# Performance work log

Measured on AMD Instinct MI355X. Metric: run time of the kernel, lower is better.

## Reference

```python
import jax, jax.numpy as jnp
import numpy as np

KMAX = 16
NEG_INF = -1e9


def setup_inputs() -> dict:
    key = jax.random.key(0)
    ks = jax.random.split(key, 8)
    B, N, H = 65536, 512, 256
    L = KMAX + 1
    actions = jax.random.randint(ks[0], (B, L), 0, N + 1)  # values in [0, N], N == STOP
    rp = jax.random.uniform(ks[1], (B, 1), dtype=jnp.float32)
    s1 = 1.0 / np.sqrt(N + 3)
    s2 = 1.0 / np.sqrt(H)
    W1 = jax.random.normal(ks[2], (N + 3, H), dtype=jnp.float32) * s1
    b1 = jax.random.normal(ks[3], (H,), dtype=jnp.float32) * 0.01
    W2 = jax.random.normal(ks[4], (H, H), dtype=jnp.float32) * s2
    b2 = jax.random.normal(ks[5], (H,), dtype=jnp.float32) * 0.01
    Wh = jax.random.normal(ks[6], (H, N + 1), dtype=jnp.float32) * s2
    bh = jax.random.normal(ks[7], (N + 1,), dtype=jnp.float32) * 0.01
    return {"actions": actions, "rp": rp, "W1": W1, "b1": b1, "W2": W2, "b2": b2, "Wh": Wh, "bh": bh}


def reference(actions, rp, W1, b1, W2, b2, Wh, bh):
    B, L = actions.shape
    N = Wh.shape[1] - 1
    f32 = rp.dtype

    def step_fn(carry, a):
        sel_mask, k_sel, step, logpf = carry  # [B,N], [B,1], [B,1], [B]
        x = jnp.concatenate([sel_mask, k_sel, step, rp], axis=-1)  # [B, N+3]
        h = jax.nn.relu(x @ W1 + b1)
        h = jax.nn.relu(h @ W2 + b2)
        logits = h @ Wh + bh  # [B, N+1]
        k = k_sel[:, 0]
        full = (k >= KMAX).astype(f32)[:, None]
        mask_assets = (1.0 - sel_mask) * (1.0 - full)  # cannot re-add or exceed Kmax
        mask_stop = (k > 0).astype(f32)[:, None]       # cannot STOP on empty set
        mask = jnp.concatenate([mask_assets, mask_stop], axis=-1)
        logits = jnp.where(mask <= 0.0, NEG_INF, logits)
        logp = jax.nn.log_softmax(logits, axis=-1)
        alive = a >= 0
        a_safe = jnp.clip(a, 0, N)
        chosen = jnp.take_along_axis(logp, a_safe[:, None], axis=-1)[:, 0]
        logpf = logpf + jnp.where(alive, chosen, 0.0)
        stop = (a == N) & alive
        add = (alive & (~stop)).astype(f32)[:, None]
        # one_hot of N/-1 is all-zero, so only valid adds update sel_mask
        upd = jax.nn.one_hot(a_safe, N, dtype=f32) * add
        sel_mask = jnp.maximum(sel_mask, upd)
        k_sel = jnp.sum(sel_mask, axis=-1, keepdims=True)
        step = step + 1.0
        return (sel_mask, k_sel, step, logpf), None

    init = (jnp.zeros((B, N), f32), jnp.zeros((B, 1), f32), jnp.zeros((B, 1), f32), jnp.zeros((B,), f32))
    (_, _, _, logpf), _ = jax.lax.scan(step_fn, init, actions.T)  # scan over L steps
    return logpf
```

## Files before the change

kernel.cpp:

```cpp
#include <hip/hip_runtime.h>


#define NEG_INF (-1000000000.0f)
#define LOG2E 1.4426950408889634f
#define LN2   0.6931471805599453f

#define A_NEW  0x400

#define HST 1040
#define HKT 2080

typedef short bf16x8 __attribute__((ext_vector_type(8)));
typedef float f32x16 __attribute__((ext_vector_type(16)));

__device__ __forceinline__ unsigned short f2bf(float x){
  unsigned int u = __float_as_uint(x);
  u = (u + 0x7FFFu + ((u >> 16) & 1u)) >> 16;
  return (unsigned short)u;
}
__device__ __forceinline__ float bf2f(unsigned short h){
  return __uint_as_float(((unsigned int)h) << 16);
}
__device__ __forceinline__ unsigned int cvt_pk_bf16(float lo, float hi){
  unsigned int r;
  asm("v_cvt_pk_bf16_f32 %0, %1, %2" : "=v"(r) : "v"(lo), "v"(hi));
  return r;
}
__device__ __forceinline__ float4 ld4bf(const unsigned short* p){
  ushort4 u = *(const ushort4*)p;
  return make_float4(bf2f(u.x), bf2f(u.y), bf2f(u.z), bf2f(u.w));
}

__global__ void prep_kernel(const float* __restrict__ W2, const float* __restrict__ Wh,
                            unsigned short* __restrict__ w2f, unsigned short* __restrict__ whf,
                            float* __restrict__ whstop){
  int id = blockIdx.x * 256 + threadIdx.x;
  if (id < 8192){
    int lane = id & 63; int tile = id >> 6;
    int ntg = tile & 7, kt = tile >> 3;
    int col = ntg * 32 + (lane & 31);
    int k0  = kt * 16 + (lane >> 5) * 8;
    unsigned int u[4];
#pragma unroll
    for (int p = 0; p < 4; ++p){
      unsigned short lo = f2bf(W2[(k0 + 2*p    ) * 256 + col]);
      unsigned short hi = f2bf(W2[(k0 + 2*p + 1) * 256 + col]);
      u[p] = (unsigned int)lo | ((unsigned int)hi << 16);
    }
    *(uint4*)(w2f + (size_t)id * 8) = make_uint4(u[0], u[1], u[2], u[3]);
  } else if (id < 24576){
    int id2 = id - 8192;
    int lane = id2 & 63; int tile = id2 >> 6;
    int ntg = tile & 15, kt = tile >> 4;
    int col = ntg * 32 + (lane & 31);
    int k0  = kt * 16 + (lane >> 5) * 8;
    unsigned int u[4];
#pragma unroll
    for (int p = 0; p < 4; ++p){
      unsigned short lo = f2bf(Wh[(k0 + 2*p    ) * 513 + col] * LOG2E);
      unsigned short hi = f2bf(Wh[(k0 + 2*p + 1) * 513 + col] * LOG2E);
      u[p] = (unsigned int)lo | ((unsigned int)hi << 16);
    }
    *(uint4*)(whf + (size_t)id2 * 8) = make_uint4(u[0], u[1], u[2], u[3]);
  } else if (id < 24832){
    int k = id - 24576;
    whstop[k] = Wh[k * 513 + 512];
  }
}

__launch_bounds__(256, 3)
__global__ void gfn_kernel(const int* __restrict__ actions, const float* __restrict__ rp,
                           const float* __restrict__ W1, const float* __restrict__ b1,
                           const float* __restrict__ b2, const float* __restrict__ bh,
                           const unsigned short* __restrict__ w2f,
                           const unsigned short* __restrict__ whf,
                           const float* __restrict__ whstop,
                           float* __restrict__ out)
{
  __shared__ alignas(16) char h[32 * HST];
  __shared__ alignas(16) unsigned short c16[1024];
  __shared__ alignas(16) unsigned int selp[16][32];
  __shared__ alignas(16) float bhl2[512];
  __shared__ alignas(16) unsigned short b2s16[256];
  __shared__ alignas(16) unsigned short whst_h[256];
  __shared__ alignas(16) unsigned short amask[18][32];
  __shared__ alignas(16) float pred[64][4];
  __shared__ alignas(16) float stopp[64];
  __shared__ alignas(16) float chosen[64];

  const int tid  = threadIdx.x;
  const int wave = tid >> 6;
  const int lane = tid & 63;
  const int ln5  = lane & 31;
  const int lg2  = lane >> 5;
  const int base = blockIdx.x * 32;

  for (int i = tid; i < 1024; i += 256){
    int rrow = i >> 8, f = i & 255;
    float v = (rrow < 3) ? W1[(512 + rrow) * 256 + f] : b1[f];
    c16[i] = f2bf(v);
  }
  b2s16[tid] = f2bf(b2[tid]);
  whst_h[tid] = f2bf(whstop[tid]);
  for (int i = tid; i < 512; i += 256){
    int pt = i >> 5, l2 = (i >> 4) & 1, r = i & 15;
    int col = pt * 32 + (r & 3) + 8 * (r >> 2) + 4 * l2;
    bhl2[i] = bh[col] * LOG2E;
  }
  const float stopbias = bh[512];
  for (int i = tid; i < 512; i += 256) ((unsigned int*)selp)[i] = 0u;
  if (tid < 64) stopp[tid] = 0.f;
  int* acts = (int*)h;
  for (int i = tid; i < 544; i += 256) acts[i] = actions[base * 17 + i];
  float logpf = 0.f;
  __syncthreads();

  if (tid < 32){
    int s = tid, k = 0;
    for (int t = 0; t < 17; ++t){
      int a = acts[s * 17 + t];
      bool alive = (a >= 0);
      bool isnew = alive && (a < 512);
      if (isnew){
        for (int u = 0; u < t; ++u) if (acts[s * 17 + u] == a){ isnew = false; break; }
      }
      int av = alive ? a : 1023;
      amask[t][s] = (unsigned short)(av | (isnew ? A_NEW : 0) | (k << 11));
      if (isnew) ++k;
    }
    amask[17][s] = (unsigned short)(1023 | (k << 11));
  }
  unsigned int Spk[16];
#pragma unroll
  for (int j = 0; j < 16; ++j) Spk[j] = 0u;
  __syncthreads();

  const int aw_base = (lane >> 1) * HST + (lane & 1) * 8 + wave * 128;
  const int br_base = lg2 * HST;
  const int bw_base = wave * 8 * HST + lg2 * 8;
  const int cr_base = lg2 * HST + ln5 * 16;
  const int rpu = __builtin_amdgcn_readfirstlane(base + wave * 8);

#pragma unroll 1
  for (int c = 0; c < 9; ++c){
    const int t = c * 2;

    {
      const float4 ck4 = ld4bf(&c16[lane * 4]);
      const float4 ct4 = ld4bf(&c16[256 + lane * 4]);
      const float4 cr4 = ld4bf(&c16[512 + lane * 4]);
      const float4 cb4 = ld4bf(&c16[768 + lane * 4]);
      float tf = (float)t;
      float c00 = cb4.x + tf * ct4.x, c01 = cb4.y + tf * ct4.y;
      float c02 = cb4.z + tf * ct4.z, c03 = cb4.w + tf * ct4.w;
#pragma unroll
      for (int s8 = 0; s8 < 8; ++s8){
        int s = wave * 8 + s8;
        float rv = rp[rpu + s8];
        int m0 = amask[t][s];
        int m1 = amask[t + 1][s];
        unsigned int pk0 = Spk[s8 * 2], pk1 = Spk[s8 * 2 + 1];
        float S0 = __uint_as_float(pk0 << 16);
        float S1 = __uint_as_float(pk0 & 0xFFFF0000u);
        float S2 = __uint_as_float(pk1 << 16);
        float S3 = __uint_as_float(pk1 & 0xFFFF0000u);
        float kf = (float)(m0 >> 11);
        float v0 = S0 + kf * ck4.x + rv * cr4.x + c00;
        float v1 = S1 + kf * ck4.y + rv * cr4.y + c01;
        float v2 = S2 + kf * ck4.z + rv * cr4.z + c02;
        float v3 = S3 + kf * ck4.w + rv * cr4.w + c03;
        *(uint2*)(h + aw_base + s8 * 16) =
            make_uint2(cvt_pk_bf16(fmaxf(v0,0.f), fmaxf(v1,0.f)),
                       cvt_pk_bf16(fmaxf(v2,0.f), fmaxf(v3,0.f)));
        float d0 = ct4.x, d1 = ct4.y, d2 = ct4.z, d3 = ct4.w;
        if (m0 & A_NEW){
          int a = m0 & 1023;
          float4 w = *(const float4*)(W1 + (size_t)a * 256 + lane * 4);
          S0 += w.x; S1 += w.y; S2 += w.z; S3 += w.w;
          d0 += w.x + ck4.x; d1 += w.y + ck4.y; d2 += w.z + ck4.z; d3 += w.w + ck4.w;
        }
        v0 += d0; v1 += d1; v2 += d2; v3 += d3;
        *(uint2*)(h + aw_base + 512 + s8 * 16) =
            make_uint2(cvt_pk_bf16(fmaxf(v0,0.f), fmaxf(v1,0.f)),
                       cvt_pk_bf16(fmaxf(v2,0.f), fmaxf(v3,0.f)));
        if (m1 & A_NEW){
          int a = m1 & 1023;
          float4 w = *(const float4*)(W1 + (size_t)a * 256 + lane * 4);
          S0 += w.x; S1 += w.y; S2 += w.z; S3 += w.w;
        }
        if ((m0 | m1) & A_NEW){
          Spk[s8 * 2]     = cvt_pk_bf16(S0, S1);
          Spk[s8 * 2 + 1] = cvt_pk_bf16(S2, S3);
        }
      }
    }
    __syncthreads();

#pragma unroll 1
    for (int q = 0; q < 2; ++q){
      const int rr = q * 32 + ln5;
      const int brq = br_base + rr * 16;
      f32x16 aB0, aB1;
#pragma unroll
      for (int i = 0; i < 16; ++i){ aB0[i] = 0.f; aB1[i] = 0.f; }
#pragma unroll 4
      for (int kt = 0; kt < 16; ++kt){
        bf16x8 sf = *(const bf16x8*)(h + brq + kt * HKT);
        bf16x8 w0 = *(const bf16x8*)(w2f + ((size_t)((kt * 8 + wave * 2    ) * 64 + lane)) * 8);
        bf16x8 w1 = *(const bf16x8*)(w2f + ((size_t)((kt * 8 + wave * 2 + 1) * 64 + lane)) * 8);
        aB0 = __builtin_amdgcn_mfma_f32_32x32x16_bf16(w0, sf, aB0, 0, 0, 0);
        aB1 = __builtin_amdgcn_mfma_f32_32x32x16_bf16(w1, sf, aB1, 0, 0, 0);
      }
      __syncthreads();
      const int bwq = bw_base + rr * 16;
      float sp = 0.f;
#pragma unroll
      for (int g = 0; g < 4; ++g){
        int f0 = wave * 64 + g * 8 + lg2 * 4;
        int f1 = f0 + 32;
        float4 bb0 = ld4bf(&b2s16[f0]);
        float4 bb1 = ld4bf(&b2s16[f1]);
        float4 ws0 = ld4bf(&whst_h[f0]);
        float4 ws1 = ld4bf(&whst_h[f1]);
        {
          float v0 = fmaxf(aB0[g*4+0] + bb0.x, 0.f), v1 = fmaxf(aB0[g*4+1] + bb0.y, 0.f);
          float v2 = fmaxf(aB0[g*4+2] + bb0.z, 0.f), v3 = fmaxf(aB0[g*4+3] + bb0.w, 0.f);
          sp += v0 * ws0.x + v1 * ws0.y + v2 * ws0.z + v3 * ws0.w;
          *(uint2*)(h + bwq + g * HST) = make_uint2(cvt_pk_bf16(v0, v1), cvt_pk_bf16(v2, v3));
        }
        {
          float v0 = fmaxf(aB1[g*4+0] + bb1.x, 0.f), v1 = fmaxf(aB1[g*4+1] + bb1.y, 0.f);
          float v2 = fmaxf(aB1[g*4+2] + bb1.z, 0.f), v3 = fmaxf(aB1[g*4+3] + bb1.w, 0.f);
          sp += v0 * ws1.x + v1 * ws1.y + v2 * ws1.z + v3 * ws1.w;
          *(uint2*)(h + bwq + (g + 4) * HST) = make_uint2(cvt_pk_bf16(v0, v1), cvt_pk_bf16(v2, v3));
        }
      }
      sp += __shfl_xor(sp, 32);
      if (lg2 == 0) atomicAdd(&stopp[rr], sp);
    }
    __syncthreads();

    {
      int mt  = amask[t][ln5];
      int mt1 = amask[t + 1][ln5];
      int av0 = mt & 1023, av1 = mt1 & 1023;
      int pa = (mt & A_NEW) ? av0 : -1;
      float sum0 = 0.f, sum1 = 0.f;
#pragma unroll 1
      for (int p = 0; p < 4; ++p){
        int pt = wave * 4 + p;
        const float* bi = &bhl2[pt * 32 + lg2 * 16];
        float4 b0_ = *(const float4*)(bi);
        float4 b1_ = *(const float4*)(bi + 4);
        float4 b2_ = *(const float4*)(bi + 8);
        float4 b3_ = *(const float4*)(bi + 12);
        f32x16 a0, a1;
        a0[0]=b0_.x; a0[1]=b0_.y; a0[2]=b0_.z; a0[3]=b0_.w;
        a0[4]=b1_.x; a0[5]=b1_.y; a0[6]=b1_.z; a0[7]=b1_.w;
        a0[8]=b2_.x; a0[9]=b2_.y; a0[10]=b2_.z; a0[11]=b2_.w;
        a0[12]=b3_.x; a0[13]=b3_.y; a0[14]=b3_.z; a0[15]=b3_.w;
        a1 = a0;
#pragma unroll 4
        for (int kt = 0; kt < 16; ++kt){
          bf16x8 f0 = *(const bf16x8*)(h + cr_base + kt * HKT);
          bf16x8 f1 = *(const bf16x8*)(h + cr_base + 512 + kt * HKT);
          bf16x8 w = *(const bf16x8*)(whf + ((size_t)((kt * 16 + pt) * 64 + lane)) * 8);
          a0 = __builtin_amdgcn_mfma_f32_32x32x16_bf16(w, f0, a0, 0, 0, 0);
          a1 = __builtin_amdgcn_mfma_f32_32x32x16_bf16(w, f1, a1, 0, 0, 0);
        }
        unsigned wsel = (selp[pt][ln5] >> (lg2 * 16)) & 0xFFFFu;
        unsigned msk0 = (mt  & 0x8000) ? 0xFFFFu : wsel;
        unsigned msk1 = (mt1 & 0x8000) ? 0xFFFFu : wsel;
        if (pa >= 0 && (pa >> 5) == pt && (((pa >> 2) & 1) == lg2))
          msk1 |= 1u << ((pa & 3) | (((pa >> 3) & 3) << 2));
        int tr0 = (av0 < 512 && (av0 >> 5) == pt && (((av0 >> 2) & 1) == lg2))
                  ? ((av0 & 3) | (((av0 >> 3) & 3) << 2)) : -1;
        int tr1 = (av1 < 512 && (av1 >> 5) == pt && (((av1 >> 2) & 1) == lg2))
                  ? ((av1 & 3) | (((av1 >> 3) & 3) << 2)) : -1;
        float cv0 = 0.f, cv1 = 0.f;
#pragma unroll
        for (int r = 0; r < 16; ++r){
          float v0 = ((msk0 >> r) & 1u) ? NEG_INF : a0[r];
          float v1 = ((msk1 >> r) & 1u) ? NEG_INF : a1[r];
          sum0 += __builtin_amdgcn_exp2f(v0);
          sum1 += __builtin_amdgcn_exp2f(v1);
          if (r == tr0) cv0 = a0[r];
          if (r == tr1) cv1 = a1[r];
        }
        if (tr0 >= 0) chosen[ln5]      = cv0;
        if (tr1 >= 0) chosen[32 + ln5] = cv1;
      }
      sum0 += __shfl_xor(sum0, 32);
      sum1 += __shfl_xor(sum1, 32);
      if (lg2 == 0){
        pred[ln5][wave]      = sum0;
        pred[32 + ln5][wave] = sum1;
      }
    }
    __syncthreads();

    if (tid < 32){
      int s = tid;
      int m0 = amask[t][s];
      int m1 = amask[t + 1][s];
      int av0 = m0 & 1023, av1 = m1 & 1023;
      int k0 = m0 >> 11, k1 = m1 >> 11;
      float stop0 = (k0 == 0) ? NEG_INF : stopp[s] + stopbias;
      float stop1 = (k1 == 0) ? NEG_INF : stopp[32 + s] + stopbias;
      {
        float tot = __expf(stop0)
                  + pred[s][0] + pred[s][1] + pred[s][2] + pred[s][3];
        float lse = __logf(tot);
        if (av0 != 1023){
          float ch;
          if (av0 == 512) ch = stop0;
          else {
            bool mskd = !(m0 & A_NEW) || (k0 >= 16);
            ch = mskd ? NEG_INF : chosen[s] * LN2;
          }
          logpf += ch - lse;
        }
        if (m0 & A_NEW){
          int pt = av0 >> 5, rf = av0 & 31;
          selp[pt][s] |= 1u << ((((rf >> 2) & 1) << 4) | (rf & 3) | (((rf >> 3) & 3) << 2));
        }
      }
      {
        int row = 32 + s;
        float tot = __expf(stop1)
                  + pred[row][0] + pred[row][1] + pred[row][2] + pred[row][3];
        float lse = __logf(tot);
        if (av1 != 1023){
          float ch;
          if (av1 == 512) ch = stop1;
          else {
            bool mskd = !(m1 & A_NEW) || (k1 >= 16);
            ch = mskd ? NEG_INF : chosen[row] * LN2;
          }
          logpf += ch - lse;
        }
        if (m1 & A_NEW){
          int pt = av1 >> 5, rf = av1 & 31;
          selp[pt][s] |= 1u << ((((rf >> 2) & 1) << 4) | (rf & 3) | (((rf >> 3) & 3) << 2));
        }
      }
      stopp[s] = 0.f; stopp[32 + s] = 0.f;
    }
    __syncthreads();
  }

  if (tid < 32) out[base + tid] = logpf;
}

extern "C" void kernel_launch(void* const* d_in, const int* in_sizes, int n_in,
                              void* d_out, int out_size, void* d_ws, size_t ws_size,
                              hipStream_t stream)
{
  const int*   actions = (const int*)d_in[0];
  const float* rp  = (const float*)d_in[1];
  const float* W1  = (const float*)d_in[2];
  const float* b1  = (const float*)d_in[3];
  const float* W2  = (const float*)d_in[4];
  const float* b2  = (const float*)d_in[5];
  const float* Wh  = (const float*)d_in[6];
  const float* bh  = (const float*)d_in[7];
  float* out = (float*)d_out;

  unsigned short* w2f = (unsigned short*)d_ws;
  unsigned short* whf = w2f + 65536;
  float* whstop = (float*)(whf + 131072);

  prep_kernel<<<97, 256, 0, stream>>>(W2, Wh, w2f, whf, whstop);
  gfn_kernel<<<2048, 256, 0, stream>>>(actions, rp, W1, b1, b2, bh, w2f, whf, whstop, out);
}
```

Baseline: 658.6 us.

## Move selection mask to registers and bf16 bias to fit four blocks per CU

Replaces the shared-memory selection bitmask with per-wave register words, updated directly by the wave that owns the chosen column. Stores the log2-scaled head bias as bf16 in shared memory instead of float. The launch bound moves from 3 to 4 blocks per CU. Together these cut LDS use so that more blocks can be resident. The risks are register spills under the tighter bound and a slight loss of bias precision.

```diff
diff --git a/kernel.cpp b/kernel.cpp
--- a/kernel.cpp
+++ b/kernel.cpp
@@ -68,7 +68,7 @@
   }
 }
 
-__launch_bounds__(256, 3)
+__launch_bounds__(256, 4)
 __global__ void gfn_kernel(const int* __restrict__ actions, const float* __restrict__ rp,
                            const float* __restrict__ W1, const float* __restrict__ b1,
                            const float* __restrict__ b2, const float* __restrict__ bh,
@@ -79,8 +79,7 @@
 {
   __shared__ alignas(16) char h[32 * HST];
   __shared__ alignas(16) unsigned short c16[1024];
-  __shared__ alignas(16) unsigned int selp[16][32];
-  __shared__ alignas(16) float bhl2[512];
+  __shared__ alignas(16) unsigned short bhl216[512];
   __shared__ alignas(16) unsigned short b2s16[256];
   __shared__ alignas(16) unsigned short whst_h[256];
   __shared__ alignas(16) unsigned short amask[18][32];
@@ -105,14 +104,14 @@
   for (int i = tid; i < 512; i += 256){
     int pt = i >> 5, l2 = (i >> 4) & 1, r = i & 15;
     int col = pt * 32 + (r & 3) + 8 * (r >> 2) + 4 * l2;
-    bhl2[i] = bh[col] * LOG2E;
+    bhl216[i] = f2bf(bh[col] * LOG2E);
   }
   const float stopbias = bh[512];
-  for (int i = tid; i < 512; i += 256) ((unsigned int*)selp)[i] = 0u;
   if (tid < 64) stopp[tid] = 0.f;
   int* acts = (int*)h;
   for (int i = tid; i < 544; i += 256) acts[i] = actions[base * 17 + i];
   float logpf = 0.f;
+  uint4 selw_r = make_uint4(0u, 0u, 0u, 0u);
   __syncthreads();
 
   if (tid < 32){
@@ -249,11 +248,11 @@
 #pragma unroll 1
       for (int p = 0; p < 4; ++p){
         int pt = wave * 4 + p;
-        const float* bi = &bhl2[pt * 32 + lg2 * 16];
-        float4 b0_ = *(const float4*)(bi);
-        float4 b1_ = *(const float4*)(bi + 4);
-        float4 b2_ = *(const float4*)(bi + 8);
-        float4 b3_ = *(const float4*)(bi + 12);
+        const unsigned short* bi = &bhl216[pt * 32 + lg2 * 16];
+        float4 b0_ = ld4bf(bi);
+        float4 b1_ = ld4bf(bi + 4);
+        float4 b2_ = ld4bf(bi + 8);
+        float4 b3_ = ld4bf(bi + 12);
         f32x16 a0, a1;
         a0[0]=b0_.x; a0[1]=b0_.y; a0[2]=b0_.z; a0[3]=b0_.w;
         a0[4]=b1_.x; a0[5]=b1_.y; a0[6]=b1_.z; a0[7]=b1_.w;
@@ -268,7 +267,10 @@
           a0 = __builtin_amdgcn_mfma_f32_32x32x16_bf16(w, f0, a0, 0, 0, 0);
           a1 = __builtin_amdgcn_mfma_f32_32x32x16_bf16(w, f1, a1, 0, 0, 0);
         }
-        unsigned wsel = (selp[pt][ln5] >> (lg2 * 16)) & 0xFFFFu;
+        unsigned wlo = (p & 1) ? selw_r.y : selw_r.x;
+        unsigned whi = (p & 1) ? selw_r.w : selw_r.z;
+        unsigned word = (p & 2) ? whi : wlo;
+        unsigned wsel = (word >> (lg2 * 16)) & 0xFFFFu;
         unsigned msk0 = (mt  & 0x8000) ? 0xFFFFu : wsel;
         unsigned msk1 = (mt1 & 0x8000) ? 0xFFFFu : wsel;
         if (pa >= 0 && (pa >> 5) == pt && (((pa >> 2) & 1) == lg2))
@@ -295,6 +297,19 @@
       if (lg2 == 0){
         pred[ln5][wave]      = sum0;
         pred[32 + ln5][wave] = sum1;
+      }
+#pragma unroll
+      for (int e = 0; e < 2; ++e){
+        int m = e ? mt1 : mt;
+        if ((m & A_NEW) && (((m & 1023) >> 7) == wave)){
+          int av = m & 1023;
+          int w2 = (av >> 5) & 3;
+          unsigned bit = 1u << ((((av >> 2) & 1) << 4) | (av & 3) | (((av >> 3) & 3) << 2));
+          if (w2 == 0) selw_r.x |= bit;
+          else if (w2 == 1) selw_r.y |= bit;
+          else if (w2 == 2) selw_r.z |= bit;
+          else selw_r.w |= bit;
+        }
       }
     }
     __syncthreads();
@@ -320,10 +335,6 @@
           }
           logpf += ch - lse;
         }
-        if (m0 & A_NEW){
-          int pt = av0 >> 5, rf = av0 & 31;
-          selp[pt][s] |= 1u << ((((rf >> 2) & 1) << 4) | (rf & 3) | (((rf >> 3) & 3) << 2));
-        }
       }
       {
         int row = 32 + s;
@@ -339,10 +350,6 @@
           }
           logpf += ch - lse;
         }
-        if (m1 & A_NEW){
-          int pt = av1 >> 5, rf = av1 & 31;
-          selp[pt][s] |= 1u << ((((rf >> 2) & 1) << 4) | (rf & 3) | (((rf >> 3) & 3) << 2));
-        }
       }
       stopp[s] = 0.f; stopp[32 + s] = 0.f;
     }
```

Result: faster. 618.6 us (-6.1%).
